# Kernel tuning notes

Hardware: AMD Instinct MI355X
Metric: run time of the kernel (lower is better)

Reference implementation:

```python
import jax, jax.numpy as jnp
import numpy as np

N_NODES = 100_000
N_EDGES = 1_600_000
N_GRAPHS = 32
D_IN = 64
D_H1 = 64
D_H2 = 64
D_OUT = 10


def setup_inputs() -> dict:
    key = jax.random.key(0)
    ks = jax.random.split(key, 6)
    x = jax.random.normal(ks[0], (N_NODES, D_IN), dtype=jnp.float32)
    edge_index = jax.random.randint(ks[1], (2, N_EDGES), 0, N_NODES, dtype=jnp.int32)
    edge_weight = jax.random.uniform(ks[2], (N_EDGES,), dtype=jnp.float32)
    # deterministic sorted graph assignment: every one of the 32 graphs nonempty
    batch = ((jnp.arange(N_NODES) * N_GRAPHS) // N_NODES).astype(jnp.int32)
    W1 = jax.random.normal(ks[3], (D_IN, D_H1), dtype=jnp.float32) * 0.1
    b1 = jnp.zeros((D_H1,), dtype=jnp.float32)
    W2 = jax.random.normal(ks[4], (D_H1, D_H2), dtype=jnp.float32) * 0.1
    b2 = jnp.zeros((D_H2,), dtype=jnp.float32)
    Wlin = jax.random.normal(ks[5], (D_H2, D_OUT), dtype=jnp.float32) * 0.1
    blin = jnp.zeros((D_OUT,), dtype=jnp.float32)
    return {"x": x, "edge_index": edge_index, "edge_weight": edge_weight,
            "batch": batch, "W1": W1, "b1": b1, "W2": W2, "b2": b2,
            "Wlin": Wlin, "blin": blin}


def _gcn_norm(edge_index, edge_weight, n_nodes):
    """GCNConv(improved=True) normalization: add self-loops with weight 2.0,
    then norm_e = deg(dst)^-1/2 * w_e * deg(src)^-1/2."""
    loop = jnp.arange(n_nodes, dtype=edge_index.dtype)
    src = jnp.concatenate([edge_index[0], loop])
    dst = jnp.concatenate([edge_index[1], loop])
    w = jnp.concatenate([edge_weight, jnp.full((n_nodes,), 2.0, edge_weight.dtype)])
    deg = jax.ops.segment_sum(w, dst, num_segments=n_nodes)
    dinv = jnp.where(deg > 0, jax.lax.rsqrt(deg), 0.0)
    norm = dinv[src] * w * dinv[dst]
    return src, dst, norm


def _gcn_conv(h, W, b, src, dst, norm, n_nodes):
    hw = h @ W                                   # [N, d_out] transform first
    msg = hw[src] * norm[:, None]                # gather + scale  [E+N, d_out]
    return jax.ops.segment_sum(msg, dst, num_segments=n_nodes) + b


def reference(x, edge_index, edge_weight, batch, W1, b1, W2, b2, Wlin, blin):
    n = x.shape[0]
    src, dst, norm = _gcn_norm(edge_index, edge_weight, n)
    h = jax.nn.relu(_gcn_conv(x, W1, b1, src, dst, norm, n))
    h = jax.nn.relu(_gcn_conv(h, W2, b2, src, dst, norm, n))
    pooled = jax.ops.segment_max(h, batch, num_segments=N_GRAPHS)  # [G, d_h2]
    return pooled @ Wlin + blin
```

## Files before the change

kernel.cpp:

```cpp
#include <hip/hip_runtime.h>

#define N_NODES 100000
#define N_GRAPHS 32
#define N_EDGES 1600000
#define NODES_PER_GRAPH 3125
#define D 64
#define DOUT 10
#define CAP 64
#define PARTS 8
#define PART_NODES 12500
#define NCHUNK 782
#define CHUNK_EDGES 2048
#define EDGE_BLOCKS (PARTS * NCHUNK)
#define GEMM_BLOCKS 6250
#define WQ 32767.0f

__device__ __forceinline__ unsigned short f2bf(float x) {
    unsigned u = __float_as_uint(x);
    u += 0x7FFFu + ((u >> 16) & 1u);
    return (unsigned short)(u >> 16);
}
__device__ __forceinline__ float bf2f(unsigned short h) {
    return __uint_as_float((unsigned)h << 16);
}

__global__ void k_init(int* cnt, unsigned int* pooled) {
    int i = blockIdx.x * blockDim.x + threadIdx.x;
    if (i < N_NODES) cnt[i] = 0;
    if (i < N_GRAPHS * D) pooled[i] = 0u;
}

__global__ void k_fill_gemm(const int* __restrict__ src, const int* __restrict__ dst,
                            const float* __restrict__ w, int* cnt,
                            unsigned int* __restrict__ bucket,
                            const float* __restrict__ X, const float* __restrict__ W,
                            unsigned short* __restrict__ Y) {
    __shared__ float4 Ws[64 * 16];
    if (blockIdx.x < EDGE_BLOCKS) {
        int p = blockIdx.x & 7;
        int chunk = blockIdx.x >> 3;
        int base = chunk * CHUNK_EDGES;
        int lo = p * PART_NODES, hi = lo + PART_NODES;
#pragma unroll
        for (int j = 0; j < 8; ++j) {
            int e = base + j * 256 + threadIdx.x;
            if (e < N_EDGES) {
                int d = dst[e];
                if (d >= lo && d < hi) {
                    int pos = atomicAdd(&cnt[d], 1);
                    if (pos < CAP) {
                        unsigned int wq = (unsigned int)(w[e] * WQ + 0.5f);
                        bucket[d * CAP + pos] = ((unsigned int)src[e] << 15) | wq;
                    }
                }
            }
        }
    } else {
        int t = threadIdx.x;
        const float4* W4 = (const float4*)W;
        for (int i = t; i < 1024; i += 256) Ws[i] = W4[i];
        __syncthreads();
        int row = (blockIdx.x - EDGE_BLOCKS) * 16 + (t >> 4);
        int c4 = t & 15;
        const float4* xr4 = (const float4*)(X + (size_t)row * D);
        float4 acc = {0.f, 0.f, 0.f, 0.f};
#pragma unroll
        for (int k4 = 0; k4 < 16; ++k4) {
            float4 xv = xr4[k4];
            float4 w0 = Ws[(k4 * 4 + 0) * 16 + c4];
            float4 w1 = Ws[(k4 * 4 + 1) * 16 + c4];
            float4 w2 = Ws[(k4 * 4 + 2) * 16 + c4];
            float4 w3 = Ws[(k4 * 4 + 3) * 16 + c4];
            acc.x += xv.x * w0.x + xv.y * w1.x + xv.z * w2.x + xv.w * w3.x;
            acc.y += xv.x * w0.y + xv.y * w1.y + xv.z * w2.y + xv.w * w3.y;
            acc.z += xv.x * w0.z + xv.y * w1.z + xv.z * w2.z + xv.w * w3.z;
            acc.w += xv.x * w0.w + xv.y * w1.w + xv.z * w2.w + xv.w * w3.w;
        }
        ushort4 o;
        o.x = f2bf(acc.x); o.y = f2bf(acc.y); o.z = f2bf(acc.z); o.w = f2bf(acc.w);
        ((ushort4*)Y)[(size_t)row * 16 + c4] = o;
    }
}

__global__ void k_deg(const int* __restrict__ cnt, const unsigned int* __restrict__ bucket,
                      float* __restrict__ dinv) {
    int node = blockIdx.x * 4 + (threadIdx.x >> 6);
    int lane = threadIdx.x & 63;
    int c = cnt[node];
    if (c > CAP) c = CAP;
    float wv = 0.0f;
    if (lane < c) wv = (float)(bucket[node * CAP + lane] & 32767u);
#pragma unroll
    for (int off = 1; off < 64; off <<= 1) wv += __shfl_xor(wv, off);
    if (lane == 0) dinv[node] = rsqrtf(2.0f + wv * (1.0f / WQ));
}

__global__ void k_gemm64v(const float* __restrict__ X, const float* __restrict__ W,
                          unsigned short* __restrict__ Y) {
    __shared__ float4 Ws[64 * 16];
    int t = threadIdx.x;
    const float4* W4 = (const float4*)W;
    for (int i = t; i < 1024; i += 256) Ws[i] = W4[i];
    __syncthreads();
    int row = blockIdx.x * 16 + (t >> 4);
    int c4 = t & 15;
    const float4* xr4 = (const float4*)(X + (size_t)row * D);
    float4 acc = {0.f, 0.f, 0.f, 0.f};
#pragma unroll
    for (int k4 = 0; k4 < 16; ++k4) {
        float4 xv = xr4[k4];
        float4 w0 = Ws[(k4 * 4 + 0) * 16 + c4];
        float4 w1 = Ws[(k4 * 4 + 1) * 16 + c4];
        float4 w2 = Ws[(k4 * 4 + 2) * 16 + c4];
        float4 w3 = Ws[(k4 * 4 + 3) * 16 + c4];
        acc.x += xv.x * w0.x + xv.y * w1.x + xv.z * w2.x + xv.w * w3.x;
        acc.y += xv.x * w0.y + xv.y * w1.y + xv.z * w2.y + xv.w * w3.y;
        acc.z += xv.x * w0.z + xv.y * w1.z + xv.z * w2.z + xv.w * w3.z;
        acc.w += xv.x * w0.w + xv.y * w1.w + xv.z * w2.w + xv.w * w3.w;
    }
    ushort4 o;
    o.x = f2bf(acc.x); o.y = f2bf(acc.y); o.z = f2bf(acc.z); o.w = f2bf(acc.w);
    ((ushort4*)Y)[(size_t)row * 16 + c4] = o;
}

__global__ void k_gather_bf(const int* __restrict__ cnt, const unsigned int* __restrict__ bucket,
                            const ushort4* __restrict__ hwb, const float* __restrict__ dinv,
                            const float* __restrict__ b, float4* __restrict__ out4) {
    int node = blockIdx.x * 4 + (threadIdx.x >> 6);
    int lane = threadIdx.x & 63;
    int g = lane >> 4, p = lane & 15;
    int end = cnt[node];
    if (end > CAP) end = CAP;
    float dvd = dinv[node];
    float wsc = dvd * (1.0f / WQ);
    const unsigned int* bk = bucket + node * CAP;
    float4 acc = {0.f, 0.f, 0.f, 0.f};
    if (g == 0) {
        float s = 2.0f * dvd * dvd;
        ushort4 u = hwb[(size_t)node * 16 + p];
        acc.x = bf2f(u.x) * s; acc.y = bf2f(u.y) * s;
        acc.z = bf2f(u.z) * s; acc.w = bf2f(u.w) * s;
    }
#define GATHER_ROUND(J)                                                      \
    {                                                                        \
        int e = g + 4 * (J);                                                 \
        bool v = e < end;                                                    \
        unsigned int be = bk[v ? e : 0];                                     \
        int s = v ? (int)(be >> 15) : 0;                                     \
        float nrm = v ? dinv[s] * (float)(be & 32767u) * wsc : 0.0f;         \
        ushort4 u = hwb[(size_t)s * 16 + p];                                 \
        acc.x += bf2f(u.x) * nrm; acc.y += bf2f(u.y) * nrm;                  \
        acc.z += bf2f(u.z) * nrm; acc.w += bf2f(u.w) * nrm;                  \
    }
    GATHER_ROUND(0) GATHER_ROUND(1) GATHER_ROUND(2) GATHER_ROUND(3)
    if (end > 16) {
        GATHER_ROUND(4) GATHER_ROUND(5) GATHER_ROUND(6) GATHER_ROUND(7)
    }
    if (end > 32) {
        for (int e = 32 + g; e < end; e += 4) {
            unsigned int be = bk[e];
            int s = (int)(be >> 15);
            float nrm = dinv[s] * (float)(be & 32767u) * wsc;
            ushort4 u = hwb[(size_t)s * 16 + p];
            acc.x += bf2f(u.x) * nrm; acc.y += bf2f(u.y) * nrm;
            acc.z += bf2f(u.z) * nrm; acc.w += bf2f(u.w) * nrm;
        }
    }
#undef GATHER_ROUND
    acc.x += __shfl_xor(acc.x, 16); acc.y += __shfl_xor(acc.y, 16);
    acc.z += __shfl_xor(acc.z, 16); acc.w += __shfl_xor(acc.w, 16);
    acc.x += __shfl_xor(acc.x, 32); acc.y += __shfl_xor(acc.y, 32);
    acc.z += __shfl_xor(acc.z, 32); acc.w += __shfl_xor(acc.w, 32);
    if (g == 0) {
        float4 bb = ((const float4*)b)[p];
        float4 r;
        r.x = fmaxf(acc.x + bb.x, 0.f);
        r.y = fmaxf(acc.y + bb.y, 0.f);
        r.z = fmaxf(acc.z + bb.z, 0.f);
        r.w = fmaxf(acc.w + bb.w, 0.f);
        out4[(size_t)node * 16 + p] = r;
    }
}

__global__ void k_pool(const float* __restrict__ h, unsigned int* pooled) {
    __shared__ float s[256];
    int g = blockIdx.x >> 3;
    int slice = blockIdx.x & 7;
    int t = threadIdx.x;
    int f = t & 63, r = t >> 6;
    float m = 0.0f;
    size_t base = (size_t)g * NODES_PER_GRAPH;
    for (int i = slice * 4 + r; i < NODES_PER_GRAPH; i += 32)
        m = fmaxf(m, h[(base + i) * D + f]);
    s[t] = m;
    __syncthreads();
    if (t < 128) s[t] = fmaxf(s[t], s[t + 128]);
    __syncthreads();
    if (t < 64) atomicMax(&pooled[g * D + t], __float_as_uint(fmaxf(s[t], s[t + 64])));
}

__global__ void k_final(const float* __restrict__ pooled, const float* __restrict__ Wlin,
                        const float* __restrict__ blin, float* __restrict__ out) {
    int t = threadIdx.x;
    if (t < N_GRAPHS * DOUT) {
        int g = t / DOUT, o = t % DOUT;
        float acc = blin[o];
#pragma unroll
        for (int f = 0; f < D; ++f) acc += pooled[g * D + f] * Wlin[f * DOUT + o];
        out[t] = acc;
    }
}

extern "C" void kernel_launch(void* const* d_in, const int* in_sizes, int n_in,
                              void* d_out, int out_size, void* d_ws, size_t ws_size,
                              hipStream_t stream) {
    const float* x     = (const float*)d_in[0];
    const int*   ei    = (const int*)d_in[1];
    const int*   src   = ei;
    const int*   dst   = ei + N_EDGES;
    const float* ew    = (const float*)d_in[2];
    const float* W1    = (const float*)d_in[4];
    const float* b1    = (const float*)d_in[5];
    const float* W2    = (const float*)d_in[6];
    const float* b2    = (const float*)d_in[7];
    const float* Wlin  = (const float*)d_in[8];
    const float* blin  = (const float*)d_in[9];
    float* out = (float*)d_out;

    unsigned int* bucket = (unsigned int*)d_ws;
    float* h1     = (float*)(bucket + (size_t)N_NODES * CAP);
    unsigned short* hwA = (unsigned short*)(h1 + (size_t)N_NODES * D);
    unsigned short* hwB = hwA + (size_t)N_NODES * D;
    float* dinv   = (float*)(hwB + (size_t)N_NODES * D);
    float* pooled = dinv + N_NODES;
    int*   cnt    = (int*)(pooled + N_GRAPHS * D);
    float* agg    = h1;

    const int B = 256;
    int gN = (N_NODES + B - 1) / B;

    k_init<<<gN, B, 0, stream>>>(cnt, (unsigned int*)pooled);
    k_fill_gemm<<<EDGE_BLOCKS + GEMM_BLOCKS, B, 0, stream>>>(src, dst, ew, cnt, bucket, x, W1, hwA);
    k_deg<<<N_NODES / 4, B, 0, stream>>>(cnt, bucket, dinv);

    k_gather_bf<<<N_NODES / 4, B, 0, stream>>>(cnt, bucket, (const ushort4*)hwA, dinv, b1, (float4*)h1);
    k_gemm64v<<<GEMM_BLOCKS, B, 0, stream>>>(h1, W2, hwB);
    k_gather_bf<<<N_NODES / 4, B, 0, stream>>>(cnt, bucket, (const ushort4*)hwB, dinv, b2, (float4*)agg);

    k_pool<<<N_GRAPHS * 8, B, 0, stream>>>(agg, (unsigned int*)pooled);
    k_final<<<1, 320, 0, stream>>>(pooled, Wlin, blin, out);
}
```

Measured before the change: 373.2 us.

## Widen gather to 16-byte bf16 loads, store layer-2 output as bf16, split pooling

The gather kernel now has each lane load 8 bf16 features (uint4) rather than 4, with 8 edge groups per node and two edges unrolled per iteration to raise memory-level parallelism. The second-layer output is written as bf16 into a new buffer, halving the bytes the pooling kernel must read. Pooling is split into 16 slices per graph instead of 8. Storing h2 as bf16 adds rounding before the max-pool, and the wider lanes hold more registers.

```diff
diff --git a/kernel.cpp b/kernel.cpp
--- a/kernel.cpp
+++ b/kernel.cpp
@@ -14,6 +14,7 @@
 #define EDGE_BLOCKS (PARTS * NCHUNK)
 #define GEMM_BLOCKS 6250
 #define WQ 32767.0f
+#define POOL_SLICES 16
 
 __device__ __forceinline__ unsigned short f2bf(float x) {
     unsigned u = __float_as_uint(x);
@@ -23,6 +24,8 @@
 __device__ __forceinline__ float bf2f(unsigned short h) {
     return __uint_as_float((unsigned)h << 16);
 }
+__device__ __forceinline__ float bflo(unsigned u) { return __uint_as_float(u << 16); }
+__device__ __forceinline__ float bfhi(unsigned u) { return __uint_as_float(u & 0xFFFF0000u); }
 
 __global__ void k_init(int* cnt, unsigned int* pooled) {
     int i = blockIdx.x * blockDim.x + threadIdx.x;
@@ -123,75 +126,104 @@
     ((ushort4*)Y)[(size_t)row * 16 + c4] = o;
 }
 
-__global__ void k_gather_bf(const int* __restrict__ cnt, const unsigned int* __restrict__ bucket,
-                            const ushort4* __restrict__ hwb, const float* __restrict__ dinv,
-                            const float* __restrict__ b, float4* __restrict__ out4) {
-    int node = blockIdx.x * 4 + (threadIdx.x >> 6);
-    int lane = threadIdx.x & 63;
-    int g = lane >> 4, p = lane & 15;
-    int end = cnt[node];
-    if (end > CAP) end = CAP;
-    float dvd = dinv[node];
-    float wsc = dvd * (1.0f / WQ);
-    const unsigned int* bk = bucket + node * CAP;
-    float4 acc = {0.f, 0.f, 0.f, 0.f};
+#define GATHER_BODY                                                              \
+    int node = blockIdx.x * 4 + (threadIdx.x >> 6);                              \
+    int lane = threadIdx.x & 63;                                                 \
+    int g = lane >> 3, q = lane & 7;                                             \
+    int end = cnt[node];                                                         \
+    if (end > CAP) end = CAP;                                                    \
+    float dvd = dinv[node];                                                      \
+    float wsc = dvd * (1.0f / WQ);                                               \
+    const unsigned int* bk = bucket + node * CAP;                                \
+    float a0=0.f,a1=0.f,a2=0.f,a3=0.f,a4=0.f,a5=0.f,a6=0.f,a7=0.f;               \
+    if (g == 0) {                                      \
+        float s = 2.0f * dvd * dvd;                                              \
+        uint4 u = hw8[(size_t)node * 8 + q];                                     \
+        a0 = bflo(u.x)*s; a1 = bfhi(u.x)*s; a2 = bflo(u.y)*s; a3 = bfhi(u.y)*s;  \
+        a4 = bflo(u.z)*s; a5 = bfhi(u.z)*s; a6 = bflo(u.w)*s; a7 = bfhi(u.w)*s;  \
+    }                                                                            \
+    int e = g;                                                                   \
+    for (; e + 8 < end; e += 16) {                                               \
+        unsigned int e0 = bk[e];                                                 \
+        unsigned int e1 = bk[e + 8];                                             \
+        int s0 = e0 >> 15, s1 = e1 >> 15;                                        \
+        float d0 = dinv[s0], d1 = dinv[s1];                                      \
+        uint4 u0 = hw8[(size_t)s0 * 8 + q];                                      \
+        uint4 u1 = hw8[(size_t)s1 * 8 + q];                                      \
+        float n0 = d0 * (float)(e0 & 32767u) * wsc;                              \
+        float n1 = d1 * (float)(e1 & 32767u) * wsc;                              \
+        a0 += bflo(u0.x)*n0 + bflo(u1.x)*n1; a1 += bfhi(u0.x)*n0 + bfhi(u1.x)*n1;\
+        a2 += bflo(u0.y)*n0 + bflo(u1.y)*n1; a3 += bfhi(u0.y)*n0 + bfhi(u1.y)*n1;\
+        a4 += bflo(u0.z)*n0 + bflo(u1.z)*n1; a5 += bfhi(u0.z)*n0 + bfhi(u1.z)*n1;\
+        a6 += bflo(u0.w)*n0 + bflo(u1.w)*n1; a7 += bfhi(u0.w)*n0 + bfhi(u1.w)*n1;\
+    }                                                                            \
+    for (; e < end; e += 8) {                                                    \
+        unsigned int ee = bk[e];                                                 \
+        int s = ee >> 15;                                                        \
+        float nrm = dinv[s] * (float)(ee & 32767u) * wsc;                        \
+        uint4 u = hw8[(size_t)s * 8 + q];                                        \
+        a0 += bflo(u.x)*nrm; a1 += bfhi(u.x)*nrm;                                \
+        a2 += bflo(u.y)*nrm; a3 += bfhi(u.y)*nrm;                                \
+        a4 += bflo(u.z)*nrm; a5 += bfhi(u.z)*nrm;                                \
+        a6 += bflo(u.w)*nrm; a7 += bfhi(u.w)*nrm;                                \
+    }                                                                            \
+                            \
+    a0 += __shfl_xor(a0, 8);  a1 += __shfl_xor(a1, 8);                           \
+    a2 += __shfl_xor(a2, 8);  a3 += __shfl_xor(a3, 8);                           \
+    a4 += __shfl_xor(a4, 8);  a5 += __shfl_xor(a5, 8);                           \
+    a6 += __shfl_xor(a6, 8);  a7 += __shfl_xor(a7, 8);                           \
+    a0 += __shfl_xor(a0, 16); a1 += __shfl_xor(a1, 16);                          \
+    a2 += __shfl_xor(a2, 16); a3 += __shfl_xor(a3, 16);                          \
+    a4 += __shfl_xor(a4, 16); a5 += __shfl_xor(a5, 16);                          \
+    a6 += __shfl_xor(a6, 16); a7 += __shfl_xor(a7, 16);                          \
+    a0 += __shfl_xor(a0, 32); a1 += __shfl_xor(a1, 32);                          \
+    a2 += __shfl_xor(a2, 32); a3 += __shfl_xor(a3, 32);                          \
+    a4 += __shfl_xor(a4, 32); a5 += __shfl_xor(a5, 32);                          \
+    a6 += __shfl_xor(a6, 32); a7 += __shfl_xor(a7, 32);
+
+__global__ void k_gather8_f32(const int* __restrict__ cnt, const unsigned int* __restrict__ bucket,
+                              const uint4* __restrict__ hw8, const float* __restrict__ dinv,
+                              const float* __restrict__ b, float4* __restrict__ out4) {
+    GATHER_BODY
     if (g == 0) {
-        float s = 2.0f * dvd * dvd;
-        ushort4 u = hwb[(size_t)node * 16 + p];
-        acc.x = bf2f(u.x) * s; acc.y = bf2f(u.y) * s;
-        acc.z = bf2f(u.z) * s; acc.w = bf2f(u.w) * s;
-    }
-#define GATHER_ROUND(J)                                                      \
-    {                                                                        \
-        int e = g + 4 * (J);                                                 \
-        bool v = e < end;                                                    \
-        unsigned int be = bk[v ? e : 0];                                     \
-        int s = v ? (int)(be >> 15) : 0;                                     \
-        float nrm = v ? dinv[s] * (float)(be & 32767u) * wsc : 0.0f;         \
-        ushort4 u = hwb[(size_t)s * 16 + p];                                 \
-        acc.x += bf2f(u.x) * nrm; acc.y += bf2f(u.y) * nrm;                  \
-        acc.z += bf2f(u.z) * nrm; acc.w += bf2f(u.w) * nrm;                  \
-    }
-    GATHER_ROUND(0) GATHER_ROUND(1) GATHER_ROUND(2) GATHER_ROUND(3)
-    if (end > 16) {
-        GATHER_ROUND(4) GATHER_ROUND(5) GATHER_ROUND(6) GATHER_ROUND(7)
-    }
-    if (end > 32) {
-        for (int e = 32 + g; e < end; e += 4) {
-            unsigned int be = bk[e];
-            int s = (int)(be >> 15);
-            float nrm = dinv[s] * (float)(be & 32767u) * wsc;
-            ushort4 u = hwb[(size_t)s * 16 + p];
-            acc.x += bf2f(u.x) * nrm; acc.y += bf2f(u.y) * nrm;
-            acc.z += bf2f(u.z) * nrm; acc.w += bf2f(u.w) * nrm;
-        }
-    }
-#undef GATHER_ROUND
-    acc.x += __shfl_xor(acc.x, 16); acc.y += __shfl_xor(acc.y, 16);
-    acc.z += __shfl_xor(acc.z, 16); acc.w += __shfl_xor(acc.w, 16);
-    acc.x += __shfl_xor(acc.x, 32); acc.y += __shfl_xor(acc.y, 32);
-    acc.z += __shfl_xor(acc.z, 32); acc.w += __shfl_xor(acc.w, 32);
+        float4 b0 = ((const float4*)b)[2 * q];
+        float4 b1 = ((const float4*)b)[2 * q + 1];
+        float4 r0, r1;
+        r0.x = fmaxf(a0 + b0.x, 0.f); r0.y = fmaxf(a1 + b0.y, 0.f);
+        r0.z = fmaxf(a2 + b0.z, 0.f); r0.w = fmaxf(a3 + b0.w, 0.f);
+        r1.x = fmaxf(a4 + b1.x, 0.f); r1.y = fmaxf(a5 + b1.y, 0.f);
+        r1.z = fmaxf(a6 + b1.z, 0.f); r1.w = fmaxf(a7 + b1.w, 0.f);
+        out4[(size_t)node * 16 + 2 * q] = r0;
+        out4[(size_t)node * 16 + 2 * q + 1] = r1;
+    }
+}
+
+__global__ void k_gather8_bf16(const int* __restrict__ cnt, const unsigned int* __restrict__ bucket,
+                               const uint4* __restrict__ hw8, const float* __restrict__ dinv,
+                               const float* __restrict__ b, uint4* __restrict__ outb) {
+    GATHER_BODY
     if (g == 0) {
-        float4 bb = ((const float4*)b)[p];
-        float4 r;
-        r.x = fmaxf(acc.x + bb.x, 0.f);
-        r.y = fmaxf(acc.y + bb.y, 0.f);
-        r.z = fmaxf(acc.z + bb.z, 0.f);
-        r.w = fmaxf(acc.w + bb.w, 0.f);
-        out4[(size_t)node * 16 + p] = r;
-    }
-}
-
-__global__ void k_pool(const float* __restrict__ h, unsigned int* pooled) {
+        float4 b0 = ((const float4*)b)[2 * q];
+        float4 b1 = ((const float4*)b)[2 * q + 1];
+        uint4 r;
+        r.x = (unsigned)f2bf(fmaxf(a0 + b0.x, 0.f)) | ((unsigned)f2bf(fmaxf(a1 + b0.y, 0.f)) << 16);
+        r.y = (unsigned)f2bf(fmaxf(a2 + b0.z, 0.f)) | ((unsigned)f2bf(fmaxf(a3 + b0.w, 0.f)) << 16);
+        r.z = (unsigned)f2bf(fmaxf(a4 + b1.x, 0.f)) | ((unsigned)f2bf(fmaxf(a5 + b1.y, 0.f)) << 16);
+        r.w = (unsigned)f2bf(fmaxf(a6 + b1.z, 0.f)) | ((unsigned)f2bf(fmaxf(a7 + b1.w, 0.f)) << 16);
+        outb[(size_t)node * 8 + q] = r;
+    }
+}
+
+__global__ void k_pool(const unsigned short* __restrict__ h, unsigned int* pooled) {
     __shared__ float s[256];
-    int g = blockIdx.x >> 3;
-    int slice = blockIdx.x & 7;
+    int g = blockIdx.x / POOL_SLICES;
+    int slice = blockIdx.x % POOL_SLICES;
     int t = threadIdx.x;
     int f = t & 63, r = t >> 6;
     float m = 0.0f;
     size_t base = (size_t)g * NODES_PER_GRAPH;
-    for (int i = slice * 4 + r; i < NODES_PER_GRAPH; i += 32)
-        m = fmaxf(m, h[(base + i) * D + f]);
+    for (int i = slice * 4 + r; i < NODES_PER_GRAPH; i += 4 * POOL_SLICES)
+        m = fmaxf(m, bf2f(h[(base + i) * D + f]));
     s[t] = m;
     __syncthreads();
     if (t < 128) s[t] = fmaxf(s[t], s[t + 128]);
@@ -231,10 +263,10 @@
     float* h1     = (float*)(bucket + (size_t)N_NODES * CAP);
     unsigned short* hwA = (unsigned short*)(h1 + (size_t)N_NODES * D);
     unsigned short* hwB = hwA + (size_t)N_NODES * D;
-    float* dinv   = (float*)(hwB + (size_t)N_NODES * D);
+    unsigned short* h2  = hwB + (size_t)N_NODES * D;
+    float* dinv   = (float*)(h2 + (size_t)N_NODES * D);
     float* pooled = dinv + N_NODES;
     int*   cnt    = (int*)(pooled + N_GRAPHS * D);
-    float* agg    = h1;
 
     const int B = 256;
     int gN = (N_NODES + B - 1) / B;
@@ -243,10 +275,10 @@
     k_fill_gemm<<<EDGE_BLOCKS + GEMM_BLOCKS, B, 0, stream>>>(src, dst, ew, cnt, bucket, x, W1, hwA);
     k_deg<<<N_NODES / 4, B, 0, stream>>>(cnt, bucket, dinv);
 
-    k_gather_bf<<<N_NODES / 4, B, 0, stream>>>(cnt, bucket, (const ushort4*)hwA, dinv, b1, (float4*)h1);
+    k_gather8_f32<<<N_NODES / 4, B, 0, stream>>>(cnt, bucket, (const uint4*)hwA, dinv, b1, (float4*)h1);
     k_gemm64v<<<GEMM_BLOCKS, B, 0, stream>>>(h1, W2, hwB);
-    k_gather_bf<<<N_NODES / 4, B, 0, stream>>>(cnt, bucket, (const ushort4*)hwB, dinv, b2, (float4*)agg);
-
-    k_pool<<<N_GRAPHS * 8, B, 0, stream>>>(agg, (unsigned int*)pooled);
+    k_gather8_bf16<<<N_NODES / 4, B, 0, stream>>>(cnt, bucket, (const uint4*)hwB, dinv, b2, (uint4*)h2);
+
+    k_pool<<<N_GRAPHS * POOL_SLICES, B, 0, stream>>>(h2, (unsigned int*)pooled);
     k_final<<<1, 320, 0, stream>>>(pooled, Wlin, blin, out);
 }
```

After: 321.9 us. 1.16x faster.
